# Kernel optimization log

Hardware: AMD Instinct MI355X
Metric: run time of the kernel (lower is better)

The kernel has to match this reference:

```python
import jax, jax.numpy as jnp
import numpy as np

NUM_HEADS = 8
TOPK = 16


def setup_inputs() -> dict:
    key = jax.random.key(0)
    ks = jax.random.split(key, 13)
    B, C, H, W = 2, 512, 64, 64
    Hu, Wu = H // 2, W // 2
    hd = C // NUM_HEADS
    n = lambda k, shape, s=1.0: jax.random.normal(k, shape, dtype=jnp.float32) * s
    return {
        "x": n(ks[0], (B, C, H, W)),
        "upper_feat": n(ks[1], (B, C, Hu, Wu)),
        "gumbel": jax.random.gumbel(ks[2], (B, NUM_HEADS, Hu * Wu), dtype=jnp.float32),
        # 1x1 convs (Conv2d + folded eval-mode BN => weight matrix + bias)
        "q_w": n(ks[3], (C, C), 0.02), "q_b": n(ks[4], (C,), 0.02),
        "kv_w": n(ks[5], (2 * C, C), 0.02), "kv_b": n(ks[6], (2 * C,), 0.02),
        "proj_w": n(ks[7], (C, C), 0.02), "proj_b": n(ks[8], (C,), 0.02),
        # depthwise 7x7 PE conv (groups = C)
        "pe_w": n(ks[9], (C, 1, 7, 7), 0.02), "pe_b": n(ks[10], (C,), 0.02),
        # gate conv1d kernel_size=1: [head_dim, 2*head_dim]
        "gate_w": n(ks[11], (hd, 2 * hd), 0.02), "gate_b": n(ks[12], (hd,), 0.02),
    }


def reference(x, upper_feat, gumbel, q_w, q_b, kv_w, kv_b, proj_w, proj_b,
              pe_w, pe_b, gate_w, gate_b):
    B, C, H, W = x.shape
    hd = C // NUM_HEADS
    Hu, Wu = upper_feat.shape[2], upper_feat.shape[3]
    N, Nu = H * W, Hu * Wu
    scale = hd ** -0.5

    def conv1x1(t, w, b):
        return jnp.einsum('bchw,oc->bohw', t, w) + b[None, :, None, None]

    # coarse attention: q from x, k/v from upper_feat
    q = conv1x1(x, q_w, q_b).reshape(B, NUM_HEADS, hd, N).transpose(0, 1, 3, 2)          # [B,h,N,d]
    kv = conv1x1(upper_feat, kv_w, kv_b).reshape(B, NUM_HEADS, 2 * hd, Nu).transpose(0, 1, 3, 2)
    k, v = kv[..., :hd], kv[..., hd:]                                                    # [B,h,Nu,d]
    sim = jnp.einsum('bhnd,bhmd->bhnm', q, k) * scale                                    # [B,h,N,Nu]
    attn = jax.nn.softmax(sim, axis=-1)
    coarse = jnp.einsum('bhnm,bhmd->bhnd', attn, v)                                      # [B,h,N,d]

    # fine branch: kv from x, top-k token selection via gumbel-softmax scores
    f_kv = conv1x1(x, kv_w, kv_b).reshape(B, NUM_HEADS, 2 * hd, N).transpose(0, 1, 3, 2)
    f_k, f_v = f_kv[..., :hd], f_kv[..., hd:]                                            # [B,h,N,d]

    # heat: channel-mean of x, adaptive-avg-pooled 2x2 to upper resolution (no grad)
    heat = jax.lax.stop_gradient(
        x.mean(axis=1).reshape(B, Hu, 2, Wu, 2).mean(axis=(2, 4)).reshape(B, Nu))
    global_sim = sim.mean(axis=2) * heat[:, None, :]                                     # [B,h,Nu]
    soft_weights = jax.nn.softmax(global_sim + gumbel, axis=-1)
    _, idx = jax.lax.top_k(soft_weights, TOPK)                                           # [B,h,K]

    # map each selected upper-token to its 2x2 block of x-tokens
    h_idx = (idx // Wu) * 2
    w_idx = (idx % Wu) * 2
    idx_full = jnp.concatenate(
        [(h_idx + dh) * W + (w_idx + dw) for dh in range(2) for dw in range(2)], axis=-1)  # [B,h,4K]

    topk_k = jnp.take_along_axis(f_k, idx_full[..., None], axis=2)                       # [B,h,4K,d]
    topk_v = jnp.take_along_axis(f_v, idx_full[..., None], axis=2)
    fine = jax.nn.softmax(jnp.einsum('bhnd,bhmd->bhnm', q, topk_k) * scale, axis=-1)
    refined = jnp.einsum('bhnm,bhmd->bhnd', fine, topk_v)                                # [B,h,N,d]

    # gated fusion (conv1d kernel_size=1 == per-token linear over 2d channels)
    fusion = jnp.concatenate([coarse, refined], axis=-1)                                 # [B,h,N,2d]
    gate = jax.nn.sigmoid(jnp.einsum('bhnc,oc->bhno', fusion, gate_w) + gate_b)
    out = gate * refined + (1.0 - gate) * coarse                                         # [B,h,N,d]

    x_out = out.transpose(0, 1, 3, 2).reshape(B, C, H, W)

    # positional encoding: depthwise 7x7 conv on v, bilinear upsample to (H,W)
    v_rs = v.transpose(0, 1, 3, 2).reshape(B, C, Hu, Wu)
    v_pe = jax.lax.conv_general_dilated(
        v_rs, pe_w, (1, 1), ((3, 3), (3, 3)), feature_group_count=C,
        dimension_numbers=('NCHW', 'OIHW', 'NCHW')) + pe_b[None, :, None, None]
    v_pe = jax.image.resize(v_pe, (B, C, H, W), method='bilinear')

    return conv1x1(x_out + v_pe, proj_w, proj_b)
```

## Files before the change

kernel.cpp:

```cpp
#include <hip/hip_runtime.h>
#include <hip/hip_bf16.h>
#include <cstdint>

typedef __hip_bfloat16 bf16;
typedef unsigned short u16;
typedef __attribute__((ext_vector_type(8))) short bf16x8;
typedef __attribute__((ext_vector_type(4))) float f32x4;

static __device__ __forceinline__ float bs2f(u16 s) {
  unsigned int u = ((unsigned int)s) << 16;
  float f;
  __builtin_memcpy(&f, &u, 4);
  return f;
}
static __device__ __forceinline__ u16 f2bs(float f) {
  bf16 h = __float2bfloat16(f);
  u16 s;
  __builtin_memcpy(&s, &h, 2);
  return s;
}
static __device__ __forceinline__ float ldf(const void* p, size_t i, int f32) {
  return f32 ? ((const float*)p)[i] : bs2f(((const u16*)p)[i]);
}

__global__ __launch_bounds__(256) void detect_dtype(const uint4* __restrict__ xs,
                                                    int* __restrict__ flag) {
  int i = blockIdx.x * 256 + threadIdx.x;
  uint4 v = xs[i];
  bool hit = false;
#pragma unroll
  for (int j = 0; j < 4; ++j) {
    unsigned w = (j == 0) ? v.x : (j == 1) ? v.y : (j == 2) ? v.z : v.w;
    if ((w & 0x7F80u) == 0x7F80u) hit = true;
    if ((w & 0x7F800000u) == 0x7F800000u) hit = true;
  }
  unsigned long long mask = __ballot(hit);
  if (mask != 0ull && (threadIdx.x & 63) == 0) atomicOr(flag, 1);
}

__global__ __launch_bounds__(256) void prep_gate(
    const void* __restrict__ gate_w, const void* __restrict__ gate_b,
    u16* __restrict__ gwb, float* __restrict__ gbf,
    const int* __restrict__ dtf) {
  const int f32 = *dtf;
  int t = threadIdx.x;
  for (int i = t; i < 8192; i += 256)
    gwb[i] = f32 ? f2bs(((const float*)gate_w)[i]) : ((const u16*)gate_w)[i];
  if (t < 64) gbf[t] = ldf(gate_b, t, f32);
}

__global__ __launch_bounds__(256) void transpose_bf16(
    const void* __restrict__ src, u16* __restrict__ dst, int N,
    float* __restrict__ heat, const int* __restrict__ dtf) {
  const int f32 = *dtf;
  const int b = blockIdx.z, n0 = blockIdx.x * 64, c0 = blockIdx.y * 64;
  const int t = threadIdx.x;
  __shared__ __align__(16) u16 tile[64][72];
#pragma unroll
  for (int j = 0; j < 2; ++j) {
    int cc = (t >> 3) + j * 32;
    int nn = (t & 7) * 8;
    u16 tmp[8];
    if (f32) {
      const float* s4 = (const float*)src + ((size_t)(b * 512 + c0 + cc)) * N + n0 + nn;
#pragma unroll
      for (int u = 0; u < 8; ++u) tmp[u] = f2bs(s4[u]);
    } else {
      *reinterpret_cast<uint4*>(tmp) = *reinterpret_cast<const uint4*>(
          (const u16*)src + ((size_t)(b * 512 + c0 + cc)) * N + n0 + nn);
    }
    *reinterpret_cast<uint4*>(&tile[cc][nn]) = *reinterpret_cast<const uint4*>(tmp);
  }
  __syncthreads();
  if (heat != nullptr && t < 32) {
    float s = 0.f;
#pragma unroll 8
    for (int cc = 0; cc < 64; ++cc)
      s += bs2f(tile[cc][2 * t]) + bs2f(tile[cc][2 * t + 1]);
    int y = blockIdx.x;
    atomicAdd(&heat[b * 1024 + (y >> 1) * 32 + t], s);
  }
#pragma unroll
  for (int j = 0; j < 2; ++j) {
    int nn = (t >> 3) + j * 32;
    int cc0 = (t & 7) * 8;
    u16 tmp[8];
#pragma unroll
    for (int u = 0; u < 8; ++u) tmp[u] = tile[cc0 + u][nn];
    *reinterpret_cast<uint4*>(&dst[((size_t)b * N + n0 + nn) * 512 + c0 + cc0]) =
        *reinterpret_cast<const uint4*>(tmp);
  }
}

template<int MODE>
__global__ __launch_bounds__(256) void gemm128(
    const u16* __restrict__ A, const void* __restrict__ W,
    const void* __restrict__ bias, u16* __restrict__ o0,
    void* __restrict__ ob, float* __restrict__ qsum, int M,
    const int* __restrict__ dtf) {
  const int f32 = *dtf;
  const int b = blockIdx.z, m0 = blockIdx.x * 128, oo0 = blockIdx.y * 64;
  const int t = threadIdx.x, w = t >> 6, lane = t & 63;
  const int quad = lane >> 4, c = lane & 15;
  __shared__ __align__(16) u16 As[128][72];
  __shared__ __align__(16) u16 Ws[64][72];
  f32x4 acc[2][4];
#pragma unroll
  for (int nt = 0; nt < 2; ++nt)
#pragma unroll
    for (int ot = 0; ot < 4; ++ot) acc[nt][ot] = (f32x4){0.f, 0.f, 0.f, 0.f};
  const u16* Ab = A + (size_t)b * M * 512;
  const int arow = t >> 1, acol = (t & 1) * 32;
  const int wrow = t >> 2, wcol = (t & 3) * 16;

  for (int k0 = 0; k0 < 512; k0 += 64) {
    __syncthreads();
    {
      const u16* ga = Ab + (size_t)(m0 + arow) * 512 + k0 + acol;
      uint4* ad = reinterpret_cast<uint4*>(&As[arow][acol]);
      const uint4* gs = reinterpret_cast<const uint4*>(ga);
      ad[0] = gs[0]; ad[1] = gs[1]; ad[2] = gs[2]; ad[3] = gs[3];
      if (f32) {
        const float* gw = (const float*)W + (size_t)(oo0 + wrow) * 512 + k0 + wcol;
#pragma unroll
        for (int e = 0; e < 16; ++e) Ws[wrow][wcol + e] = f2bs(gw[e]);
      } else {
        const u16* gw = (const u16*)W + (size_t)(oo0 + wrow) * 512 + k0 + wcol;
        *reinterpret_cast<uint4*>(&Ws[wrow][wcol])     = *reinterpret_cast<const uint4*>(gw);
        *reinterpret_cast<uint4*>(&Ws[wrow][wcol + 8]) = *reinterpret_cast<const uint4*>(gw + 8);
      }
    }
    __syncthreads();
#pragma unroll
    for (int ks = 0; ks < 2; ++ks) {
      bf16x8 av[2];
      av[0] = *reinterpret_cast<const bf16x8*>(&As[w * 32 + c][ks * 32 + quad * 8]);
      av[1] = *reinterpret_cast<const bf16x8*>(&As[w * 32 + 16 + c][ks * 32 + quad * 8]);
#pragma unroll
      for (int ot = 0; ot < 4; ++ot) {
        bf16x8 wv = *reinterpret_cast<const bf16x8*>(&Ws[ot * 16 + c][ks * 32 + quad * 8]);
#pragma unroll
        for (int nt = 0; nt < 2; ++nt) {
          if (MODE == 3)
            acc[nt][ot] = __builtin_amdgcn_mfma_f32_16x16x32_bf16(wv, av[nt], acc[nt][ot], 0, 0, 0);
          else
            acc[nt][ot] = __builtin_amdgcn_mfma_f32_16x16x32_bf16(av[nt], wv, acc[nt][ot], 0, 0, 0);
        }
      }
    }
  }

  if (MODE == 0) {
    const int h = oo0 >> 6, bh = b * 8 + h;
#pragma unroll
    for (int ot = 0; ot < 4; ++ot) {
      int o = oo0 + ot * 16 + c;
      int d = o & 63;
      float bv = ldf(bias, o, f32);
      float qs = 0.f;
#pragma unroll
      for (int nt = 0; nt < 2; ++nt)
#pragma unroll
        for (int r = 0; r < 4; ++r) {
          int m = m0 + w * 32 + nt * 16 + quad * 4 + r;
          u16 val = f2bs(acc[nt][ot][r] + bv);
          o0[((size_t)bh * M + m) * 64 + d] = val;
          qs += bs2f(val);
        }
      qs += __shfl_xor(qs, 16, 64);
      qs += __shfl_xor(qs, 32, 64);
      if (quad == 0) atomicAdd(&qsum[bh * 64 + d], qs);
    }
  } else {
#pragma unroll
    for (int ot = 0; ot < 4; ++ot)
#pragma unroll
      for (int r = 0; r < 4; ++r) {
        int o = oo0 + ot * 16 + quad * 4 + r;
        float bv = ldf(bias, o, f32);
#pragma unroll
        for (int nt = 0; nt < 2; ++nt) {
          int m = m0 + w * 32 + nt * 16 + c;
          float val = acc[nt][ot][r] + bv;
          size_t oi_ = ((size_t)(b * 512 + o)) * M + m;
          if (f32) ((float*)ob)[oi_] = val;
          else     ((u16*)ob)[oi_] = f2bs(val);
        }
      }
  }
}

__global__ __launch_bounds__(256) void gemm_kv(
    const u16* __restrict__ A, const void* __restrict__ W,
    const void* __restrict__ bias, u16* __restrict__ kb, u16* __restrict__ vTb,
    int M, const int* __restrict__ dtf) {
  const int f32 = *dtf;
  const int b = blockIdx.z, m0 = blockIdx.x * 64, oo0 = blockIdx.y * 64;
  const int t = threadIdx.x, w = t >> 6, lane = t & 63;
  const int quad = lane >> 4, c = lane & 15;
  __shared__ __align__(16) u16 As[64][72];
  __shared__ __align__(16) u16 Ws[64][72];
  f32x4 acc[4];
#pragma unroll
  for (int ot = 0; ot < 4; ++ot) acc[ot] = (f32x4){0.f, 0.f, 0.f, 0.f};
  const u16* Ab = A + (size_t)b * M * 512;
  const int srow = t >> 2, scol = (t & 3) * 16;

  for (int k0 = 0; k0 < 512; k0 += 64) {
    __syncthreads();
    {
      const u16* ga = Ab + (size_t)(m0 + srow) * 512 + k0 + scol;
      *reinterpret_cast<uint4*>(&As[srow][scol])     = *reinterpret_cast<const uint4*>(ga);
      *reinterpret_cast<uint4*>(&As[srow][scol + 8]) = *reinterpret_cast<const uint4*>(ga + 8);
      if (f32) {
        const float* gw = (const float*)W + (size_t)(oo0 + srow) * 512 + k0 + scol;
#pragma unroll
        for (int e = 0; e < 16; ++e) Ws[srow][scol + e] = f2bs(gw[e]);
      } else {
        const u16* gw = (const u16*)W + (size_t)(oo0 + srow) * 512 + k0 + scol;
        *reinterpret_cast<uint4*>(&Ws[srow][scol])     = *reinterpret_cast<const uint4*>(gw);
        *reinterpret_cast<uint4*>(&Ws[srow][scol + 8]) = *reinterpret_cast<const uint4*>(gw + 8);
      }
    }
    __syncthreads();
#pragma unroll
    for (int ks = 0; ks < 2; ++ks) {
      bf16x8 av = *reinterpret_cast<const bf16x8*>(&As[w * 16 + c][ks * 32 + quad * 8]);
#pragma unroll
      for (int ot = 0; ot < 4; ++ot) {
        bf16x8 wv = *reinterpret_cast<const bf16x8*>(&Ws[ot * 16 + c][ks * 32 + quad * 8]);
        acc[ot] = __builtin_amdgcn_mfma_f32_16x16x32_bf16(av, wv, acc[ot], 0, 0, 0);
      }
    }
  }

#pragma unroll
  for (int ot = 0; ot < 4; ++ot) {
    int o = oo0 + ot * 16 + c;
    float bv = ldf(bias, o, f32);
    int hh = o >> 7, jj = o & 127;
#pragma unroll
    for (int r = 0; r < 4; ++r) {
      int m = m0 + w * 16 + quad * 4 + r;
      u16 val = f2bs(acc[ot][r] + bv);
      if (jj < 64) kb[((size_t)(b * 8 + hh) * M + m) * 64 + jj] = val;
      else         vTb[((size_t)(b * 8 + hh) * 64 + (jj & 63)) * M + m] = val;
    }
  }
}

__global__ __launch_bounds__(256) void topk_kernel(
    const float* __restrict__ qsum, const u16* __restrict__ k,
    const float* __restrict__ heat, const void* __restrict__ gumbel,
    int* __restrict__ posb, const int* __restrict__ dtf) {
  const int f32 = *dtf;
  int bh = blockIdx.x, b = bh >> 3, t = threadIdx.x;
  __shared__ float qs[64];
  __shared__ float s[1024];
  __shared__ float rv[256];
  __shared__ int   ri[256];
  if (t < 64) qs[t] = qsum[bh * 64 + t];
  __syncthreads();
  for (int j = 0; j < 4; ++j) {
    int m = t + j * 256;
    const u16* kr = k + ((size_t)bh * 1024 + m) * 64;
    float dot = 0.f;
    for (int d = 0; d < 64; ++d) dot += qs[d] * bs2f(kr[d]);
    s[m] = dot * (0.125f / 4096.0f) * (heat[b * 1024 + m] * (1.0f / 2048.0f)) +
           ldf(gumbel, (size_t)bh * 1024 + m, f32);
  }
  __syncthreads();
  for (int it = 0; it < 16; ++it) {
    float bv = -1e30f; int bi = 0x7fffffff;
    for (int j = 0; j < 4; ++j) {
      int m = t + j * 256; float vv = s[m];
      if (vv > bv || (vv == bv && m < bi)) { bv = vv; bi = m; }
    }
    rv[t] = bv; ri[t] = bi; __syncthreads();
    for (int off = 128; off; off >>= 1) {
      if (t < off) {
        if (rv[t + off] > rv[t] || (rv[t + off] == rv[t] && ri[t + off] < ri[t])) {
          rv[t] = rv[t + off]; ri[t] = ri[t + off];
        }
      }
      __syncthreads();
    }
    if (t == 0) {
      int mi = ri[0]; s[mi] = -1e30f;
      int hy = (mi >> 5) * 2, wx = (mi & 31) * 2;
      posb[bh * 64 + it]      = hy * 64 + wx;
      posb[bh * 64 + 16 + it] = hy * 64 + wx + 1;
      posb[bh * 64 + 32 + it] = (hy + 1) * 64 + wx;
      posb[bh * 64 + 48 + it] = (hy + 1) * 64 + wx + 1;
    }
    __syncthreads();
  }
}

__global__ __launch_bounds__(256) void gather_kv_mfma(
    const u16* __restrict__ xT, const void* __restrict__ kv_w,
    const void* __restrict__ kv_b, const int* __restrict__ posb,
    u16* __restrict__ tkb, u16* __restrict__ tvTb,
    const int* __restrict__ dtf) {
  const int f32 = *dtf;
  const int bh = blockIdx.x, b = bh >> 3, h = bh & 7;
  const int half = blockIdx.y;
  const int t = threadIdx.x, w = t >> 6, lane = t & 63;
  const int quad = lane >> 4, c = lane & 15;
  __shared__ int pos[64];
  __shared__ __align__(16) u16 As[64][72];
  __shared__ __align__(16) u16 Ws[64][72];
  if (t < 64) pos[t] = posb[bh * 64 + t];
  __syncthreads();
  const int obase = h * 128 + half * 64;
  const int srow = t >> 2, scol = (t & 3) * 16;
  const int arow = pos[srow];
  f32x4 acc[4];
#pragma unroll
  for (int ot = 0; ot < 4; ++ot) acc[ot] = (f32x4){0.f, 0.f, 0.f, 0.f};

  for (int k0 = 0; k0 < 512; k0 += 64) {
    __syncthreads();
    {
      const u16* ga = xT + ((size_t)b * 4096 + arow) * 512 + k0 + scol;
      *reinterpret_cast<uint4*>(&As[srow][scol])     = *reinterpret_cast<const uint4*>(ga);
      *reinterpret_cast<uint4*>(&As[srow][scol + 8]) = *reinterpret_cast<const uint4*>(ga + 8);
      if (f32) {
        const float* gw = (const float*)kv_w + (size_t)(obase + srow) * 512 + k0 + scol;
#pragma unroll
        for (int e = 0; e < 16; ++e) Ws[srow][scol + e] = f2bs(gw[e]);
      } else {
        const u16* gw = (const u16*)kv_w + (size_t)(obase + srow) * 512 + k0 + scol;
        *reinterpret_cast<uint4*>(&Ws[srow][scol])     = *reinterpret_cast<const uint4*>(gw);
        *reinterpret_cast<uint4*>(&Ws[srow][scol + 8]) = *reinterpret_cast<const uint4*>(gw + 8);
      }
    }
    __syncthreads();
#pragma unroll
    for (int ks = 0; ks < 2; ++ks) {
      bf16x8 av = *reinterpret_cast<const bf16x8*>(&As[w * 16 + c][ks * 32 + quad * 8]);
#pragma unroll
      for (int ot = 0; ot < 4; ++ot) {
        bf16x8 wv = *reinterpret_cast<const bf16x8*>(&Ws[ot * 16 + c][ks * 32 + quad * 8]);
        acc[ot] = __builtin_amdgcn_mfma_f32_16x16x32_bf16(av, wv, acc[ot], 0, 0, 0);
      }
    }
  }

#pragma unroll
  for (int ot = 0; ot < 4; ++ot) {
    int d = ot * 16 + c;
    float bv = ldf(kv_b, obase + d, f32);
#pragma unroll
    for (int r = 0; r < 4; ++r) {
      int m = w * 16 + quad * 4 + r;
      u16 val = f2bs(acc[ot][r] + bv);
      if (half) tvTb[((size_t)bh * 64 + d) * 64 + m] = val;
      else      tkb[((size_t)bh * 64 + m) * 64 + d] = val;
    }
  }
}

__global__ __launch_bounds__(256) void dwconv_kernel(
    const u16* __restrict__ vT, const void* __restrict__ pe_w,
    const void* __restrict__ pe_b, u16* __restrict__ vpe,
    const int* __restrict__ dtf) {
  const int f32 = *dtf;
  int bc = blockIdx.x;
  int b = bc >> 9, c = bc & 511;
  int h = c >> 6, d = c & 63;
  int t = threadIdx.x;
  __shared__ float img[1024];
  __shared__ float wts[49];
  const u16* base = vT + ((size_t)(b * 8 + h) * 64 + d) * 1024;
  if (t < 128) {
    uint4 v4 = reinterpret_cast<const uint4*>(base)[t];
    u16 tmp[8];
    *reinterpret_cast<uint4*>(tmp) = v4;
#pragma unroll
    for (int e = 0; e < 8; ++e) img[t * 8 + e] = bs2f(tmp[e]);
  }
  if (t < 49) wts[t] = ldf(pe_w, c * 49 + t, f32);
  float bias = ldf(pe_b, c, f32);
  __syncthreads();
  for (int i = t; i < 1024; i += 256) {
    int y = i >> 5, xx = i & 31;
    float a = 0.f;
#pragma unroll
    for (int ky = 0; ky < 7; ++ky) {
      int yy = y + ky - 3;
      if ((unsigned)yy >= 32u) continue;
#pragma unroll
      for (int kx = 0; kx < 7; ++kx) {
        int xc = xx + kx - 3;
        if ((unsigned)xc >= 32u) continue;
        a += img[yy * 32 + xc] * wts[ky * 7 + kx];
      }
    }
    vpe[(size_t)bc * 1024 + i] = f2bs(a + bias);
  }
}

__global__ __launch_bounds__(256) void attn_fused(
    const u16* __restrict__ q, const u16* __restrict__ k,
    const u16* __restrict__ vT, const u16* __restrict__ tkb,
    const u16* __restrict__ tvTb, const u16* __restrict__ gwb,
    const float* __restrict__ gbf, const u16* __restrict__ vpe,
    u16* __restrict__ xsT) {
  const int bh = blockIdx.y, b = bh >> 3, h = bh & 7;
  const int bx = blockIdx.x;
  const int n0 = bx * 128;
  const int t = threadIdx.x, w = t >> 6, lane = t & 63;
  const int quad = lane >> 4, c = lane & 15;

  __shared__ __align__(16) u16 lds[18432];
  u16* Ks = lds;
  u16* Vt = lds + 4608;
  u16* Ps = lds + 9216;

  bf16x8 bq[2][2];
#pragma unroll
  for (int nt = 0; nt < 2; ++nt) {
    const u16* qr = q + ((size_t)bh * 4096 + n0 + w * 32 + nt * 16 + c) * 64;
    bq[nt][0] = *reinterpret_cast<const bf16x8*>(qr + quad * 8);
    bq[nt][1] = *reinterpret_cast<const bf16x8*>(qr + 32 + quad * 8);
  }
  f32x4 po[2][4];
#pragma unroll
  for (int nt = 0; nt < 2; ++nt)
#pragma unroll
    for (int dt = 0; dt < 4; ++dt) po[nt][dt] = (f32x4){0.f, 0.f, 0.f, 0.f};
  float sume[2] = {0.f, 0.f};

  const u16* kbase = k + (size_t)bh * 65536;
  const u16* vbase = vT + (size_t)bh * 65536;
  const int srow = t >> 2, scol = (t & 3) * 16;

  uint4 kr0, kr1, vr0, vr1;
  {
    const u16* gk = kbase + (size_t)srow * 64 + scol;
    kr0 = *reinterpret_cast<const uint4*>(gk);
    kr1 = *reinterpret_cast<const uint4*>(gk + 8);
    const u16* gv = vbase + (size_t)srow * 1024 + scol;
    vr0 = *reinterpret_cast<const uint4*>(gv);
    vr1 = *reinterpret_cast<const uint4*>(gv + 8);
  }

  for (int ch = 0; ch < 16; ++ch) {
    __syncthreads();
    *reinterpret_cast<uint4*>(&Ks[srow * 72 + scol])     = kr0;
    *reinterpret_cast<uint4*>(&Ks[srow * 72 + scol + 8]) = kr1;
    *reinterpret_cast<uint4*>(&Vt[srow * 72 + scol])     = vr0;
    *reinterpret_cast<uint4*>(&Vt[srow * 72 + scol + 8]) = vr1;
    __syncthreads();
    if (ch + 1 < 16) {
      const int m1 = (ch + 1) * 64;
      const u16* gk = kbase + (size_t)(m1 + srow) * 64 + scol;
      kr0 = *reinterpret_cast<const uint4*>(gk);
      kr1 = *reinterpret_cast<const uint4*>(gk + 8);
      const u16* gv = vbase + (size_t)srow * 1024 + m1 + scol;
      vr0 = *reinterpret_cast<const uint4*>(gv);
      vr1 = *reinterpret_cast<const uint4*>(gv + 8);
    }

    f32x4 st[2][4];
#pragma unroll
    for (int mt = 0; mt < 4; ++mt) {
      const u16* krow = &Ks[(mt * 16 + c) * 72];
      bf16x8 ak0 = *reinterpret_cast<const bf16x8*>(krow + quad * 8);
      bf16x8 ak1 = *reinterpret_cast<const bf16x8*>(krow + 32 + quad * 8);
#pragma unroll
      for (int nt = 0; nt < 2; ++nt) {
        f32x4 acc = (f32x4){0.f, 0.f, 0.f, 0.f};
        acc = __builtin_amdgcn_mfma_f32_16x16x32_bf16(ak0, bq[nt][0], acc, 0, 0, 0);
        acc = __builtin_amdgcn_mfma_f32_16x16x32_bf16(ak1, bq[nt][1], acc, 0, 0, 0);
        st[nt][mt] = acc;
      }
    }
#pragma unroll
    for (int nt = 0; nt < 2; ++nt) {
      float cs = 0.f;
      u16* psw = &Ps[((w * 2 + nt) * 16 + c) * 72];
#pragma unroll
      for (int mt = 0; mt < 4; ++mt) {
        float e0 = __expf(st[nt][mt][0] * 0.125f);
        float e1 = __expf(st[nt][mt][1] * 0.125f);
        float e2 = __expf(st[nt][mt][2] * 0.125f);
        float e3 = __expf(st[nt][mt][3] * 0.125f);
        cs += (e0 + e1) + (e2 + e3);
        ushort4 pw;
        pw.x = f2bs(e0); pw.y = f2bs(e1); pw.z = f2bs(e2); pw.w = f2bs(e3);
        *reinterpret_cast<ushort4*>(psw + mt * 16 + quad * 4) = pw;
      }
      cs += __shfl_xor(cs, 16, 64);
      cs += __shfl_xor(cs, 32, 64);
      sume[nt] += cs;
    }
#pragma unroll
    for (int s = 0; s < 2; ++s) {
      bf16x8 bp0 = *reinterpret_cast<const bf16x8*>(&Ps[((w * 2 + 0) * 16 + c) * 72 + s * 32 + quad * 8]);
      bf16x8 bp1 = *reinterpret_cast<const bf16x8*>(&Ps[((w * 2 + 1) * 16 + c) * 72 + s * 32 + quad * 8]);
#pragma unroll
      for (int dt = 0; dt < 4; ++dt) {
        bf16x8 av = *reinterpret_cast<const bf16x8*>(&Vt[(dt * 16 + c) * 72 + s * 32 + quad * 8]);
        po[0][dt] = __builtin_amdgcn_mfma_f32_16x16x32_bf16(av, bp0, po[0][dt], 0, 0, 0);
        po[1][dt] = __builtin_amdgcn_mfma_f32_16x16x32_bf16(av, bp1, po[1][dt], 0, 0, 0);
      }
    }
  }

  __syncthreads();
  u16* fus = lds;
  u16* vl  = lds + 8704;
  float* gbl = (float*)(lds + 15616);

  for (int idx = t; idx < 768; idx += 256) {
    int seg = idx & 3, ch2 = (idx >> 2) & 63, rr = idx >> 8;
    int vrow = bx - 1 + rr;
    vrow = vrow < 0 ? 0 : (vrow > 31 ? 31 : vrow);
    const uint4 v4 = *reinterpret_cast<const uint4*>(
        vpe + ((size_t)(b * 512 + h * 64 + ch2)) * 1024 + vrow * 32 + seg * 8);
    u16* dst = &vl[(rr * 64 + ch2) * 36 + seg * 8];
    uint2 lo, hi;
    lo.x = v4.x; lo.y = v4.y; hi.x = v4.z; hi.y = v4.w;
    *reinterpret_cast<uint2*>(dst)     = lo;
    *reinterpret_cast<uint2*>(dst + 4) = hi;
  }
  if (t < 64) gbl[t] = gbf[t];
  __syncthreads();

  for (int nt = 0; nt < 2; ++nt) {
    u16* fusw = &fus[(w * 16 + c) * 136];
    f32x4 st2[4];
#pragma unroll
    for (int mt = 0; mt < 4; ++mt) {
      f32x4 acc = (f32x4){0.f, 0.f, 0.f, 0.f};
#pragma unroll
      for (int s = 0; s < 2; ++s) {
        bf16x8 ak = *reinterpret_cast<const bf16x8*>(
            &tkb[((size_t)bh * 64 + mt * 16 + c) * 64 + s * 32 + quad * 8]);
        acc = __builtin_amdgcn_mfma_f32_16x16x32_bf16(ak, bq[nt][s], acc, 0, 0, 0);
      }
      st2[mt] = acc;
    }
    float sume2 = 0.f;
#pragma unroll
    for (int mt = 0; mt < 4; ++mt) {
      float e0 = __expf(st2[mt][0] * 0.125f);
      float e1 = __expf(st2[mt][1] * 0.125f);
      float e2 = __expf(st2[mt][2] * 0.125f);
      float e3 = __expf(st2[mt][3] * 0.125f);
      sume2 += (e0 + e1) + (e2 + e3);
      ushort4 pw;
      pw.x = f2bs(e0); pw.y = f2bs(e1); pw.z = f2bs(e2); pw.w = f2bs(e3);
      *reinterpret_cast<ushort4*>(fusw + mt * 16 + quad * 4) = pw;
    }
    sume2 += __shfl_xor(sume2, 16, 64);
    sume2 += __shfl_xor(sume2, 32, 64);
    float inv2 = 1.0f / sume2;

    f32x4 po2[4];
#pragma unroll
    for (int dt = 0; dt < 4; ++dt) po2[dt] = (f32x4){0.f, 0.f, 0.f, 0.f};
#pragma unroll
    for (int s = 0; s < 2; ++s) {
      bf16x8 bp = *reinterpret_cast<const bf16x8*>(fusw + s * 32 + quad * 8);
#pragma unroll
      for (int dt = 0; dt < 4; ++dt) {
        bf16x8 av = *reinterpret_cast<const bf16x8*>(
            &tvTb[((size_t)bh * 64 + dt * 16 + c) * 64 + s * 32 + quad * 8]);
        po2[dt] = __builtin_amdgcn_mfma_f32_16x16x32_bf16(av, bp, po2[dt], 0, 0, 0);
      }
    }

    float invc = 1.0f / sume[nt];
#pragma unroll
    for (int dt = 0; dt < 4; ++dt) {
      ushort4 cw, rw;
      cw.x = f2bs(po[nt][dt][0] * invc); cw.y = f2bs(po[nt][dt][1] * invc);
      cw.z = f2bs(po[nt][dt][2] * invc); cw.w = f2bs(po[nt][dt][3] * invc);
      rw.x = f2bs(po2[dt][0] * inv2);    rw.y = f2bs(po2[dt][1] * inv2);
      rw.z = f2bs(po2[dt][2] * inv2);    rw.w = f2bs(po2[dt][3] * inv2);
      *reinterpret_cast<ushort4*>(fusw + dt * 16 + quad * 4)      = cw;
      *reinterpret_cast<ushort4*>(fusw + 64 + dt * 16 + quad * 4) = rw;
    }

    f32x4 ga[4];
#pragma unroll
    for (int ot = 0; ot < 4; ++ot) ga[ot] = (f32x4){0.f, 0.f, 0.f, 0.f};
#pragma unroll
    for (int s = 0; s < 4; ++s) {
      bf16x8 bf = *reinterpret_cast<const bf16x8*>(fusw + s * 32 + quad * 8);
#pragma unroll
      for (int ot = 0; ot < 4; ++ot) {
        bf16x8 ag = *reinterpret_cast<const bf16x8*>(
            gwb + (ot * 16 + c) * 128 + s * 32 + quad * 8);
        ga[ot] = __builtin_amdgcn_mfma_f32_16x16x32_bf16(ag, bf, ga[ot], 0, 0, 0);
      }
    }

    const int ylocal = (w * 32 + nt * 16) >> 6;
    const int x = (w * 32 + nt * 16 + c) & 63;
    float wy0, wy1; int i0, i1;
    if (ylocal == 0) { wy0 = 0.25f; wy1 = 0.75f; i0 = (bx > 0) ? 0 : 1; i1 = 1; }
    else             { wy0 = 0.75f; wy1 = 0.25f; i0 = 1; i1 = (bx < 31) ? 2 : 1; }
    int jx = x >> 1, x0, x1; float wx0, wx1;
    if ((x & 1) == 0) { x0 = (jx > 0) ? jx - 1 : 0; x1 = jx; wx0 = 0.25f; wx1 = 0.75f; }
    else              { x0 = jx; x1 = (jx < 31) ? jx + 1 : 31; wx0 = 0.75f; wx1 = 0.25f; }
#pragma unroll
    for (int dt = 0; dt < 4; ++dt) {
      ushort4 ow;
      u16 tmp[4];
#pragma unroll
      for (int r = 0; r < 4; ++r) {
        int row = dt * 16 + quad * 4 + r;
        float ref = po2[dt][r] * inv2;
        float coar = bs2f(fusw[row]);
        float g = 1.0f / (1.0f + __expf(-(ga[dt][r] + gbl[row])));
        float vv = wy0 * (wx0 * bs2f(vl[(i0 * 64 + row) * 36 + x0]) +
                          wx1 * bs2f(vl[(i0 * 64 + row) * 36 + x1])) +
                   wy1 * (wx0 * bs2f(vl[(i1 * 64 + row) * 36 + x0]) +
                          wx1 * bs2f(vl[(i1 * 64 + row) * 36 + x1]));
        tmp[r] = f2bs(g * ref + (1.0f - g) * coar + vv);
      }
      ow.x = tmp[0]; ow.y = tmp[1]; ow.z = tmp[2]; ow.w = tmp[3];
      *reinterpret_cast<ushort4*>(fusw + dt * 16 + quad * 4) = ow;
    }

    {
      int nl = lane >> 2, cs2 = (lane & 3) * 16;
      const u16* srcrow = &fus[(w * 16 + nl) * 136 + cs2];
      u16* dst = xsT + ((size_t)b * 4096 + n0 + w * 32 + nt * 16 + nl) * 512 + h * 64 + cs2;
      *reinterpret_cast<uint4*>(dst)     = *reinterpret_cast<const uint4*>(srcrow);
      *reinterpret_cast<uint4*>(dst + 8) = *reinterpret_cast<const uint4*>(srcrow + 8);
    }
  }
}

extern "C" void kernel_launch(void* const* d_in, const int* in_sizes, int n_in,
                              void* d_out, int out_size, void* d_ws, size_t ws_size,
                              hipStream_t stream) {
  const void* x    = d_in[0];
  const void* up   = d_in[1];
  const void* gum  = d_in[2];
  const void* q_w  = d_in[3];
  const void* q_b  = d_in[4];
  const void* kv_w = d_in[5];
  const void* kv_b = d_in[6];
  const void* p_w  = d_in[7];
  const void* p_b  = d_in[8];
  const void* pe_w = d_in[9];
  const void* pe_b = d_in[10];
  const void* g_w  = d_in[11];
  const void* g_b  = d_in[12];

  float* ws    = (float*)d_ws;
  int*   dtf   = (int*)ws;
  float* qsum  = ws + 16;
  float* heat  = qsum + 1024;
  int*   posb  = (int*)(heat + 2048);
  float* gbf   = (float*)(posb + 1024);
  u16*   gwb   = (u16*)(gbf + 64);
  u16*   tkb   = gwb + 8192;
  u16*   tvTb  = tkb + 65536;
  u16*   qb    = tvTb + 65536;
  u16*   kb    = qb + 4194304;
  u16*   vTb   = kb + 1048576;
  u16*   xT    = vTb + 1048576;
  u16*   upT   = xT + 4194304;
  u16*   xsT   = upT + 1048576;
  u16*   vpe   = xsT + 4194304;

  dim3 blk(256);
  hipMemsetAsync(ws, 0, (16 + 1024 + 2048) * 4, stream);
  detect_dtype<<<dim3(64), blk, 0, stream>>>((const uint4*)x, dtf);
  prep_gate<<<dim3(1), blk, 0, stream>>>(g_w, g_b, gwb, gbf, dtf);
  transpose_bf16<<<dim3(64, 8, 2), blk, 0, stream>>>(x, xT, 4096, heat, dtf);
  transpose_bf16<<<dim3(16, 8, 2), blk, 0, stream>>>(up, upT, 1024, nullptr, dtf);
  gemm128<0><<<dim3(32, 8, 2), blk, 0, stream>>>(xT, q_w, q_b, qb, nullptr, qsum, 4096, dtf);
  gemm_kv<<<dim3(16, 16, 2), blk, 0, stream>>>(upT, kv_w, kv_b, kb, vTb, 1024, dtf);
  topk_kernel<<<dim3(16), blk, 0, stream>>>(qsum, kb, heat, gum, posb, dtf);
  gather_kv_mfma<<<dim3(16, 2), blk, 0, stream>>>(xT, kv_w, kv_b, posb, tkb, tvTb, dtf);
  dwconv_kernel<<<dim3(1024), blk, 0, stream>>>(vTb, pe_w, pe_b, vpe, dtf);
  attn_fused<<<dim3(32, 16), blk, 0, stream>>>(qb, kb, vTb, tkb, tvTb, gwb, gbf, vpe, xsT);
  gemm128<3><<<dim3(32, 8, 2), blk, 0, stream>>>(xsT, p_w, p_b, nullptr, d_out, nullptr, 4096, dtf);
}
```

Baseline: 264.7 us.

## Load K/V MFMA fragments directly from global memory, drop LDS staging

The coarse attention loop no longer stages K and V^T chunks through shared memory with two barriers per chunk. Each wave now loads its MFMA operand fragments straight from global memory (through L2/L1) and unrolls the loop by two. The intent is to remove the barriers and the LDS store/load traffic and to shrink the LDS footprint. The cost is that every wave fetches the same K/V data redundantly and the loads are less coalesced, and the explicit register prefetch of the next chunk is gone.

```diff
diff --git a/kernel.cpp b/kernel.cpp
--- a/kernel.cpp
+++ b/kernel.cpp
@@ -413,10 +413,8 @@
   const int t = threadIdx.x, w = t >> 6, lane = t & 63;
   const int quad = lane >> 4, c = lane & 15;
 
-  __shared__ __align__(16) u16 lds[18432];
-  u16* Ks = lds;
-  u16* Vt = lds + 4608;
-  u16* Ps = lds + 9216;
+  __shared__ __align__(16) u16 lds[15744];
+  u16* Ps = lds;
 
   bf16x8 bq[2][2];
 #pragma unroll
@@ -434,46 +432,33 @@
 
   const u16* kbase = k + (size_t)bh * 65536;
   const u16* vbase = vT + (size_t)bh * 65536;
-  const int srow = t >> 2, scol = (t & 3) * 16;
-
-  uint4 kr0, kr1, vr0, vr1;
-  {
-    const u16* gk = kbase + (size_t)srow * 64 + scol;
-    kr0 = *reinterpret_cast<const uint4*>(gk);
-    kr1 = *reinterpret_cast<const uint4*>(gk + 8);
-    const u16* gv = vbase + (size_t)srow * 1024 + scol;
-    vr0 = *reinterpret_cast<const uint4*>(gv);
-    vr1 = *reinterpret_cast<const uint4*>(gv + 8);
-  }
-
+
+#pragma unroll 2
   for (int ch = 0; ch < 16; ++ch) {
-    __syncthreads();
-    *reinterpret_cast<uint4*>(&Ks[srow * 72 + scol])     = kr0;
-    *reinterpret_cast<uint4*>(&Ks[srow * 72 + scol + 8]) = kr1;
-    *reinterpret_cast<uint4*>(&Vt[srow * 72 + scol])     = vr0;
-    *reinterpret_cast<uint4*>(&Vt[srow * 72 + scol + 8]) = vr1;
-    __syncthreads();
-    if (ch + 1 < 16) {
-      const int m1 = (ch + 1) * 64;
-      const u16* gk = kbase + (size_t)(m1 + srow) * 64 + scol;
-      kr0 = *reinterpret_cast<const uint4*>(gk);
-      kr1 = *reinterpret_cast<const uint4*>(gk + 8);
-      const u16* gv = vbase + (size_t)srow * 1024 + m1 + scol;
-      vr0 = *reinterpret_cast<const uint4*>(gv);
-      vr1 = *reinterpret_cast<const uint4*>(gv + 8);
+    const int m1 = ch * 64;
+    bf16x8 av[4][2];
+#pragma unroll
+    for (int dt = 0; dt < 4; ++dt) {
+      const u16* vp = vbase + (size_t)(dt * 16 + c) * 1024 + m1 + quad * 8;
+      av[dt][0] = *reinterpret_cast<const bf16x8*>(vp);
+      av[dt][1] = *reinterpret_cast<const bf16x8*>(vp + 32);
+    }
+    bf16x8 ak[4][2];
+#pragma unroll
+    for (int mt = 0; mt < 4; ++mt) {
+      const u16* kp = kbase + (size_t)(m1 + mt * 16 + c) * 64 + quad * 8;
+      ak[mt][0] = *reinterpret_cast<const bf16x8*>(kp);
+      ak[mt][1] = *reinterpret_cast<const bf16x8*>(kp + 32);
     }
 
     f32x4 st[2][4];
 #pragma unroll
     for (int mt = 0; mt < 4; ++mt) {
-      const u16* krow = &Ks[(mt * 16 + c) * 72];
-      bf16x8 ak0 = *reinterpret_cast<const bf16x8*>(krow + quad * 8);
-      bf16x8 ak1 = *reinterpret_cast<const bf16x8*>(krow + 32 + quad * 8);
 #pragma unroll
       for (int nt = 0; nt < 2; ++nt) {
         f32x4 acc = (f32x4){0.f, 0.f, 0.f, 0.f};
-        acc = __builtin_amdgcn_mfma_f32_16x16x32_bf16(ak0, bq[nt][0], acc, 0, 0, 0);
-        acc = __builtin_amdgcn_mfma_f32_16x16x32_bf16(ak1, bq[nt][1], acc, 0, 0, 0);
+        acc = __builtin_amdgcn_mfma_f32_16x16x32_bf16(ak[mt][0], bq[nt][0], acc, 0, 0, 0);
+        acc = __builtin_amdgcn_mfma_f32_16x16x32_bf16(ak[mt][1], bq[nt][1], acc, 0, 0, 0);
         st[nt][mt] = acc;
       }
     }
@@ -502,9 +487,8 @@
       bf16x8 bp1 = *reinterpret_cast<const bf16x8*>(&Ps[((w * 2 + 1) * 16 + c) * 72 + s * 32 + quad * 8]);
 #pragma unroll
       for (int dt = 0; dt < 4; ++dt) {
-        bf16x8 av = *reinterpret_cast<const bf16x8*>(&Vt[(dt * 16 + c) * 72 + s * 32 + quad * 8]);
-        po[0][dt] = __builtin_amdgcn_mfma_f32_16x16x32_bf16(av, bp0, po[0][dt], 0, 0, 0);
-        po[1][dt] = __builtin_amdgcn_mfma_f32_16x16x32_bf16(av, bp1, po[1][dt], 0, 0, 0);
+        po[0][dt] = __builtin_amdgcn_mfma_f32_16x16x32_bf16(av[dt][s], bp0, po[0][dt], 0, 0, 0);
+        po[1][dt] = __builtin_amdgcn_mfma_f32_16x16x32_bf16(av[dt][s], bp1, po[1][dt], 0, 0, 0);
       }
     }
   }
```

After: 318.5 us. +20.3%, slower.

## Store V in MFMA fragment layout and double-buffer K tiles in coarse attention

Applied to the files above, without the earlier changes.

The gemm_kv epilogue now writes V in a layout that already matches the MFMA A-operand fragments, so attn_fused loads V operands straight from global memory into registers instead of staging them through LDS. The K tile is double-buffered in LDS, which removes one barrier per chunk, and the dwconv kernel is adapted to read the new V layout. This cuts LDS traffic and synchronisation in the main attention loop. In exchange, the epilogue scatters its writes and attention depends on global and L2 latency for V loads, with no prefetch ahead of use.

```diff
diff --git a/kernel.cpp b/kernel.cpp
--- a/kernel.cpp
+++ b/kernel.cpp
@@ -192,7 +192,7 @@
 
 __global__ __launch_bounds__(256) void gemm_kv(
     const u16* __restrict__ A, const void* __restrict__ W,
-    const void* __restrict__ bias, u16* __restrict__ kb, u16* __restrict__ vTb,
+    const void* __restrict__ bias, u16* __restrict__ kb, u16* __restrict__ v2,
     int M, const int* __restrict__ dtf) {
   const int f32 = *dtf;
   const int b = blockIdx.z, m0 = blockIdx.x * 64, oo0 = blockIdx.y * 64;
@@ -243,8 +243,13 @@
     for (int r = 0; r < 4; ++r) {
       int m = m0 + w * 16 + quad * 4 + r;
       u16 val = f2bs(acc[ot][r] + bv);
-      if (jj < 64) kb[((size_t)(b * 8 + hh) * M + m) * 64 + jj] = val;
-      else         vTb[((size_t)(b * 8 + hh) * 64 + (jj & 63)) * M + m] = val;
+      if (jj < 64) {
+        kb[((size_t)(b * 8 + hh) * M + m) * 64 + jj] = val;
+      } else {
+        int d = jj & 63;
+        v2[((((size_t)(b * 8 + hh) * 16 + (m >> 6)) * 2 + ((m >> 5) & 1)) * 4 + (d >> 4)) * 512
+           + (((m >> 3) & 3) * 16 + (d & 15)) * 8 + (m & 7)] = val;
+      }
     }
   }
 }
@@ -362,19 +367,22 @@
 }
 
 __global__ __launch_bounds__(256) void dwconv_kernel(
-    const u16* __restrict__ vT, const void* __restrict__ pe_w,
+    const u16* __restrict__ v2, const void* __restrict__ pe_w,
     const void* __restrict__ pe_b, u16* __restrict__ vpe,
     const int* __restrict__ dtf) {
   const int f32 = *dtf;
   int bc = blockIdx.x;
   int b = bc >> 9, c = bc & 511;
   int h = c >> 6, d = c & 63;
+  int dt = d >> 4, cc = d & 15;
   int t = threadIdx.x;
   __shared__ float img[1024];
   __shared__ float wts[49];
-  const u16* base = vT + ((size_t)(b * 8 + h) * 64 + d) * 1024;
   if (t < 128) {
-    uint4 v4 = reinterpret_cast<const uint4*>(base)[t];
+    int ch = t >> 3, s = (t >> 2) & 1, q2 = t & 3;
+    const u16* src = v2 + ((((size_t)(b * 8 + h) * 16 + ch) * 2 + s) * 4 + dt) * 512
+                        + (q2 * 16 + cc) * 8;
+    uint4 v4 = *reinterpret_cast<const uint4*>(src);
     u16 tmp[8];
     *reinterpret_cast<uint4*>(tmp) = v4;
 #pragma unroll
@@ -403,7 +411,7 @@
 
 __global__ __launch_bounds__(256) void attn_fused(
     const u16* __restrict__ q, const u16* __restrict__ k,
-    const u16* __restrict__ vT, const u16* __restrict__ tkb,
+    const u16* __restrict__ v2, const u16* __restrict__ tkb,
     const u16* __restrict__ tvTb, const u16* __restrict__ gwb,
     const float* __restrict__ gbf, const u16* __restrict__ vpe,
     u16* __restrict__ xsT) {
@@ -415,7 +423,6 @@
 
   __shared__ __align__(16) u16 lds[18432];
   u16* Ks = lds;
-  u16* Vt = lds + 4608;
   u16* Ps = lds + 9216;
 
   bf16x8 bq[2][2];
@@ -433,40 +440,39 @@
   float sume[2] = {0.f, 0.f};
 
   const u16* kbase = k + (size_t)bh * 65536;
-  const u16* vbase = vT + (size_t)bh * 65536;
+  const u16* v2base = v2 + (size_t)bh * 65536;
   const int srow = t >> 2, scol = (t & 3) * 16;
 
-  uint4 kr0, kr1, vr0, vr1;
+  uint4 kr0, kr1;
   {
     const u16* gk = kbase + (size_t)srow * 64 + scol;
     kr0 = *reinterpret_cast<const uint4*>(gk);
     kr1 = *reinterpret_cast<const uint4*>(gk + 8);
-    const u16* gv = vbase + (size_t)srow * 1024 + scol;
-    vr0 = *reinterpret_cast<const uint4*>(gv);
-    vr1 = *reinterpret_cast<const uint4*>(gv + 8);
+    *reinterpret_cast<uint4*>(&Ks[srow * 72 + scol])     = kr0;
+    *reinterpret_cast<uint4*>(&Ks[srow * 72 + scol + 8]) = kr1;
+    const u16* gk1 = kbase + (size_t)(64 + srow) * 64 + scol;
+    kr0 = *reinterpret_cast<const uint4*>(gk1);
+    kr1 = *reinterpret_cast<const uint4*>(gk1 + 8);
   }
 
   for (int ch = 0; ch < 16; ++ch) {
     __syncthreads();
-    *reinterpret_cast<uint4*>(&Ks[srow * 72 + scol])     = kr0;
-    *reinterpret_cast<uint4*>(&Ks[srow * 72 + scol + 8]) = kr1;
-    *reinterpret_cast<uint4*>(&Vt[srow * 72 + scol])     = vr0;
-    *reinterpret_cast<uint4*>(&Vt[srow * 72 + scol + 8]) = vr1;
-    __syncthreads();
-    if (ch + 1 < 16) {
-      const int m1 = (ch + 1) * 64;
-      const u16* gk = kbase + (size_t)(m1 + srow) * 64 + scol;
-      kr0 = *reinterpret_cast<const uint4*>(gk);
-      kr1 = *reinterpret_cast<const uint4*>(gk + 8);
-      const u16* gv = vbase + (size_t)srow * 1024 + m1 + scol;
-      vr0 = *reinterpret_cast<const uint4*>(gv);
-      vr1 = *reinterpret_cast<const uint4*>(gv + 8);
+    const int buf = ch & 1;
+
+    bf16x8 av[4][2];
+    {
+      const u16* v2c = v2base + (size_t)ch * 4096;
+#pragma unroll
+      for (int dt = 0; dt < 4; ++dt) {
+        av[dt][0] = *reinterpret_cast<const bf16x8*>(v2c + dt * 512 + lane * 8);
+        av[dt][1] = *reinterpret_cast<const bf16x8*>(v2c + 2048 + dt * 512 + lane * 8);
+      }
     }
 
     f32x4 st[2][4];
 #pragma unroll
     for (int mt = 0; mt < 4; ++mt) {
-      const u16* krow = &Ks[(mt * 16 + c) * 72];
+      const u16* krow = &Ks[buf * 4608 + (mt * 16 + c) * 72];
       bf16x8 ak0 = *reinterpret_cast<const bf16x8*>(krow + quad * 8);
       bf16x8 ak1 = *reinterpret_cast<const bf16x8*>(krow + 32 + quad * 8);
 #pragma unroll
@@ -477,6 +483,17 @@
         st[nt][mt] = acc;
       }
     }
+
+    if (ch + 1 < 16) {
+      *reinterpret_cast<uint4*>(&Ks[(buf ^ 1) * 4608 + srow * 72 + scol])     = kr0;
+      *reinterpret_cast<uint4*>(&Ks[(buf ^ 1) * 4608 + srow * 72 + scol + 8]) = kr1;
+      if (ch + 2 < 16) {
+        const u16* gk = kbase + (size_t)((ch + 2) * 64 + srow) * 64 + scol;
+        kr0 = *reinterpret_cast<const uint4*>(gk);
+        kr1 = *reinterpret_cast<const uint4*>(gk + 8);
+      }
+    }
+
 #pragma unroll
     for (int nt = 0; nt < 2; ++nt) {
       float cs = 0.f;
@@ -502,9 +519,8 @@
       bf16x8 bp1 = *reinterpret_cast<const bf16x8*>(&Ps[((w * 2 + 1) * 16 + c) * 72 + s * 32 + quad * 8]);
 #pragma unroll
       for (int dt = 0; dt < 4; ++dt) {
-        bf16x8 av = *reinterpret_cast<const bf16x8*>(&Vt[(dt * 16 + c) * 72 + s * 32 + quad * 8]);
-        po[0][dt] = __builtin_amdgcn_mfma_f32_16x16x32_bf16(av, bp0, po[0][dt], 0, 0, 0);
-        po[1][dt] = __builtin_amdgcn_mfma_f32_16x16x32_bf16(av, bp1, po[1][dt], 0, 0, 0);
+        po[0][dt] = __builtin_amdgcn_mfma_f32_16x16x32_bf16(av[dt][s], bp0, po[0][dt], 0, 0, 0);
+        po[1][dt] = __builtin_amdgcn_mfma_f32_16x16x32_bf16(av[dt][s], bp1, po[1][dt], 0, 0, 0);
       }
     }
   }
@@ -665,8 +681,8 @@
   u16*   tvTb  = tkb + 65536;
   u16*   qb    = tvTb + 65536;
   u16*   kb    = qb + 4194304;
-  u16*   vTb   = kb + 1048576;
-  u16*   xT    = vTb + 1048576;
+  u16*   v2b   = kb + 1048576;
+  u16*   xT    = v2b + 1048576;
   u16*   upT   = xT + 4194304;
   u16*   xsT   = upT + 1048576;
   u16*   vpe   = xsT + 4194304;
@@ -678,10 +694,10 @@
   transpose_bf16<<<dim3(64, 8, 2), blk, 0, stream>>>(x, xT, 4096, heat, dtf);
   transpose_bf16<<<dim3(16, 8, 2), blk, 0, stream>>>(up, upT, 1024, nullptr, dtf);
   gemm128<0><<<dim3(32, 8, 2), blk, 0, stream>>>(xT, q_w, q_b, qb, nullptr, qsum, 4096, dtf);
-  gemm_kv<<<dim3(16, 16, 2), blk, 0, stream>>>(upT, kv_w, kv_b, kb, vTb, 1024, dtf);
+  gemm_kv<<<dim3(16, 16, 2), blk, 0, stream>>>(upT, kv_w, kv_b, kb, v2b, 1024, dtf);
   topk_kernel<<<dim3(16), blk, 0, stream>>>(qsum, kb, heat, gum, posb, dtf);
   gather_kv_mfma<<<dim3(16, 2), blk, 0, stream>>>(xT, kv_w, kv_b, posb, tkb, tvTb, dtf);
-  dwconv_kernel<<<dim3(1024), blk, 0, stream>>>(vTb, pe_w, pe_b, vpe, dtf);
-  attn_fused<<<dim3(32, 16), blk, 0, stream>>>(qb, kb, vTb, tkb, tvTb, gwb, gbf, vpe, xsT);
+  dwconv_kernel<<<dim3(1024), blk, 0, stream>>>(v2b, pe_w, pe_b, vpe, dtf);
+  attn_fused<<<dim3(32, 16), blk, 0, stream>>>(qb, kb, v2b, tkb, tvTb, gwb, gbf, vpe, xsT);
   gemm128<3><<<dim3(32, 8, 2), blk, 0, stream>>>(xsT, p_w, p_b, nullptr, d_out, nullptr, 4096, dtf);
 }
```

Result: no change. 263.0 us (-0.7%).
